# Optimization experiments

Hardware: AMD Instinct MI355X
Metric: run time of the kernel (lower is better)

## Reference

```python
import jax, jax.numpy as jnp
import numpy as np

EMBED = 1024
HEADS = 16
HEAD_DIM = EMBED // HEADS


def setup_inputs() -> dict:
    key = jax.random.key(0)
    ks = jax.random.split(key, 7)
    B, S = 2, 2048
    return {
        "key": jax.random.normal(ks[0], (B, S, EMBED), dtype=jnp.float32),
        "query": jax.random.normal(ks[1], (B, S, EMBED), dtype=jnp.float32),
        "value": jax.random.normal(ks[2], (B, S, EMBED), dtype=jnp.float32),
        "Wk": jax.random.normal(ks[3], (EMBED, EMBED), dtype=jnp.float32) * (EMBED ** -0.5),
        "Wq": jax.random.normal(ks[4], (EMBED, EMBED), dtype=jnp.float32) * (EMBED ** -0.5),
        "Wv": jax.random.normal(ks[5], (EMBED, EMBED), dtype=jnp.float32) * (EMBED ** -0.5),
        "Wo": jax.random.normal(ks[6], (EMBED, EMBED), dtype=jnp.float32) * (EMBED ** -0.5),
        "mask": 1,
    }


def _split_heads(x):
    B, S, _ = x.shape
    return x.reshape(B, S, HEADS, HEAD_DIM).transpose(0, 2, 1, 3)  # (B,H,S,D)


def reference(key, query, value, Wk, Wq, Wv, Wo, mask):
    # torch Linear (no bias): y = x @ W.T
    k = _split_heads(key @ Wk.T)
    q = _split_heads(query @ Wq.T)
    v = _split_heads(value @ Wv.T)
    # NOTE: module scales by sqrt(embed_dims), not sqrt(head_dims)
    scale = 1.0 / jnp.sqrt(jnp.float32(EMBED))
    scores = jnp.einsum('bhqd,bhkd->bhqk', q, k) * scale  # (B,H,S,S)
    S = scores.shape[-1]
    if mask:
        # triu(full(-100000), diagonal=1).type(int) -> exactly -100000 above diag
        causal = jnp.triu(jnp.full((S, S), -100000.0, dtype=jnp.float32), k=1)
        scores = scores + causal
    attn = jax.nn.softmax(scores, axis=-1)
    out = jnp.einsum('bhqk,bhkd->bhqd', attn, v)  # (B,H,S,D)
    B = out.shape[0]
    out = out.transpose(0, 2, 1, 3).reshape(B, S, EMBED)
    return out @ Wo.T
```

## Files before the change

kernel.cpp:

```cpp
#include <hip/hip_runtime.h>
#include <hip/hip_bf16.h>

typedef unsigned short u16;
typedef __attribute__((ext_vector_type(8))) short bf16x8;
typedef __attribute__((ext_vector_type(4))) float f32x4;

#define GLDS16(g, l)                                                        \
  __builtin_amdgcn_global_load_lds(                                         \
      (const __attribute__((address_space(1))) void*)(g),                   \
      (__attribute__((address_space(3))) void*)(l), 16, 0, 0)

__device__ __forceinline__ u16 f2bf(float f) {
  union { float f; unsigned u; } v; v.f = f;
  unsigned r = v.u + 0x7FFFu + ((v.u >> 16) & 1u);
  return (u16)(r >> 16);
}

__global__ __launch_bounds__(256) void cvt_kernel(const float4* __restrict__ in,
                                                  ushort4* __restrict__ out) {
  int i = blockIdx.x * 256 + threadIdx.x;
  float4 v = in[i];
  ushort4 o;
  o.x = f2bf(v.x); o.y = f2bf(v.y); o.z = f2bf(v.z); o.w = f2bf(v.w);
  out[i] = o;
}

template <int MODE>
__device__ __forceinline__ void gemm_core(const u16* __restrict__ A,
                                          const u16* __restrict__ W,
                                          void* __restrict__ C) {
  const int K = 1024;
  __shared__ u16 lds_a[4096];
  __shared__ u16 lds_b[4096];
  const int bn = blockIdx.x, bm = blockIdx.y;
  const int tid = threadIdx.x, l = tid & 63, wid = tid >> 6;
  const int wr = wid >> 1, wc = wid & 1;
  const int l4 = l >> 4, l15 = l & 15;

  f32x4 zero4 = {0.f, 0.f, 0.f, 0.f};
  f32x4 acc[4][4];
  for (int i = 0; i < 4; ++i)
    for (int j = 0; j < 4; ++j) acc[i][j] = zero4;

  const int srow = tid >> 2, scol = (tid & 3) * 8;
  const u16* Ag = A + (bm * 128 + srow) * K + scol;
  const u16* Wg = W + (bn * 128 + srow) * K + scol;
  char* la = (char*)lds_a + wid * 1024;
  char* lb = (char*)lds_b + wid * 1024;

  for (int kt = 0; kt < K; kt += 32) {
    GLDS16(Ag + kt, la);
    GLDS16(Ag + 64 * K + kt, la + 4096);
    GLDS16(Wg + kt, lb);
    GLDS16(Wg + 64 * K + kt, lb + 4096);
    __syncthreads();
    bf16x8 af[4], bf[4];
    for (int i = 0; i < 4; ++i)
      af[i] = *(const bf16x8*)((const char*)lds_a +
                               (wr * 64 + i * 16 + l15) * 64 + l4 * 16);
    for (int j = 0; j < 4; ++j)
      bf[j] = *(const bf16x8*)((const char*)lds_b +
                               (wc * 64 + j * 16 + l15) * 64 + l4 * 16);
    for (int i = 0; i < 4; ++i)
      for (int j = 0; j < 4; ++j)
        acc[i][j] = __builtin_amdgcn_mfma_f32_16x16x32_bf16(af[i], bf[j],
                                                            acc[i][j], 0, 0, 0);
    __syncthreads();
  }

  for (int i = 0; i < 4; ++i)
    for (int j = 0; j < 4; ++j) {
      f32x4 a = acc[i][j];
      for (int r = 0; r < 4; ++r) {
        int m = bm * 128 + wr * 64 + i * 16 + l4 * 4 + r;
        int n = bn * 128 + wc * 64 + j * 16 + l15;
        if (MODE == 0) {
          int bb = m >> 11, srw = m & 2047, h = n >> 6, d = n & 63;
          ((u16*)C)[((bb * 16 + h) * 2048 + srw) * 64 + d] = f2bf(a[r]);
        } else {
          ((float*)C)[m * 1024 + n] = a[r];
        }
      }
    }
}

__global__ __launch_bounds__(256) void gemm_proj(
    const u16* __restrict__ X0, const u16* __restrict__ X1,
    const u16* __restrict__ X2, const u16* __restrict__ W0,
    const u16* __restrict__ W1, const u16* __restrict__ W2,
    u16* __restrict__ O0, u16* __restrict__ O1, u16* __restrict__ O2) {
  int z = blockIdx.z;
  const u16* A = (z == 0) ? X0 : (z == 1) ? X1 : X2;
  const u16* W = (z == 0) ? W0 : (z == 1) ? W1 : W2;
  u16* O = (z == 0) ? O0 : (z == 1) ? O1 : O2;
  gemm_core<0>(A, W, (void*)O);
}

__global__ __launch_bounds__(256) void gemm_out(const u16* __restrict__ A,
                                                const u16* __restrict__ W,
                                                float* __restrict__ C) {
  gemm_core<1>(A, W, (void*)C);
}

__global__ __launch_bounds__(256) void transpose_v(const u16* __restrict__ Vp,
                                                   u16* __restrict__ Vt) {
  const int st = blockIdx.x, bh = blockIdx.y;
  const int d = threadIdx.x & 63, sg = threadIdx.x >> 6;
  const u16* src = Vp + bh * 131072;
  u16* dst = Vt + bh * 131072;
  const int s0 = st * 64 + sg * 16;
  u16 tmp[16];
  for (int i = 0; i < 16; ++i) tmp[i] = src[(s0 + i) * 64 + d];
  ushort4* o = (ushort4*)(dst + d * 2048 + s0);
  for (int k = 0; k < 4; ++k) {
    ushort4 t4;
    t4.x = tmp[4 * k]; t4.y = tmp[4 * k + 1];
    t4.z = tmp[4 * k + 2]; t4.w = tmp[4 * k + 3];
    o[k] = t4;
  }
}

__global__ __launch_bounds__(256) void attn_kernel(const u16* __restrict__ Qp,
                                                   const u16* __restrict__ Kp,
                                                   const u16* __restrict__ Vt,
                                                   u16* __restrict__ ctx) {
  const int x = blockIdx.x, bh = blockIdx.y;
  const int tid = threadIdx.x, w = tid >> 6, l = tid & 63;
  const int l4 = l >> 4, l15 = l & 15;
  __shared__ u16 lds_p[4][1024];
  char* pw = (char*)lds_p[w];

  const u16* Qbh = Qp + bh * 131072;
  const u16* Kbh = Kp + bh * 131072;
  const u16* Vbh = Vt + bh * 131072;
  const int b = bh >> 4, h = bh & 15;
  u16* ctxb = ctx + (size_t)b * 2048 * 1024 + h * 64;

  const float SCALE2 = 0.03125f * 1.44269504f;
  const float PEN2 = 144269.5f;
  const int swz = (l15 & 7) << 4;

  for (int half = 0; half < 2; ++half) {
    const int qt = half ? (31 - x) : x;
    const int q0 = qt * 64 + w * 16;

    const u16* qb = Qbh + (q0 + l15) * 64 + l4 * 8;
    const bf16x8 bq0 = *(const bf16x8*)(qb);
    const bf16x8 bq1 = *(const bf16x8*)(qb + 32);

    f32x4 zero4 = {0.f, 0.f, 0.f, 0.f};
    f32x4 accO[4];
    for (int g = 0; g < 4; ++g) accO[g] = zero4;
    float m2 = -1.0e30f, lsum = 0.f;

    for (int t2 = 0; t2 <= qt; ++t2) {
      const int kv0 = t2 * 64;
      const u16* kb = Kbh + (kv0 + l15) * 64 + l4 * 8;
      f32x4 s[4];
      for (int g = 0; g < 4; ++g) {
        bf16x8 kf = *(const bf16x8*)(kb + g * 1024);
        s[g] = __builtin_amdgcn_mfma_f32_16x16x32_bf16(kf, bq0, zero4, 0, 0, 0);
      }
      for (int g = 0; g < 4; ++g) {
        bf16x8 kf = *(const bf16x8*)(kb + g * 1024 + 32);
        s[g] = __builtin_amdgcn_mfma_f32_16x16x32_bf16(kf, bq1, s[g], 0, 0, 0);
      }
      const u16* vb = Vbh + l15 * 2048 + kv0 + l4 * 8;
      bf16x8 vf[8];
      for (int g = 0; g < 4; ++g) {
        vf[g] = *(const bf16x8*)(vb + g * 16 * 2048);
        vf[g + 4] = *(const bf16x8*)(vb + g * 16 * 2048 + 32);
      }
      float sv[4][4];
      if (t2 == qt) {
        const int q = q0 + l15;
        for (int g = 0; g < 4; ++g)
          for (int r = 0; r < 4; ++r) {
            int kv = kv0 + g * 16 + l4 * 4 + r;
            sv[g][r] = s[g][r] * SCALE2 - (kv > q ? PEN2 : 0.f);
          }
      } else {
        for (int g = 0; g < 4; ++g)
          for (int r = 0; r < 4; ++r) sv[g][r] = s[g][r] * SCALE2;
      }
      float mx = sv[0][0];
      for (int g = 0; g < 4; ++g)
        for (int r = 0; r < 4; ++r) mx = fmaxf(mx, sv[g][r]);
      mx = fmaxf(mx, __shfl_xor(mx, 16));
      mx = fmaxf(mx, __shfl_xor(mx, 32));
      const float mnew = fmaxf(m2, mx);
      const float alpha = __builtin_exp2f(m2 - mnew);
      m2 = mnew;
      float p[4][4], rs = 0.f;
      for (int g = 0; g < 4; ++g)
        for (int r = 0; r < 4; ++r) {
          float e = __builtin_exp2f(sv[g][r] - mnew);
          p[g][r] = e;
          rs += e;
        }
      rs += __shfl_xor(rs, 16);
      rs += __shfl_xor(rs, 32);
      lsum = lsum * alpha + rs;
      float aR[4];
      for (int r = 0; r < 4; ++r) aR[r] = __shfl(alpha, l4 * 4 + r);
      for (int g = 0; g < 4; ++g) {
        f32x4 t = accO[g];
        t[0] *= aR[0]; t[1] *= aR[1]; t[2] *= aR[2]; t[3] *= aR[3];
        accO[g] = t;
      }
      for (int g = 0; g < 4; ++g) {
        ushort4 q4;
        q4.x = f2bf(p[g][0]); q4.y = f2bf(p[g][1]);
        q4.z = f2bf(p[g][2]); q4.w = f2bf(p[g][3]);
        int byte = (l15 * 128 + g * 32 + l4 * 8) ^ swz;
        *(ushort4*)(pw + byte) = q4;
      }
      bf16x8 pa0 = *(const bf16x8*)(pw + ((l15 * 128 + l4 * 16) ^ swz));
      bf16x8 pa1 = *(const bf16x8*)(pw + ((l15 * 128 + 64 + l4 * 16) ^ swz));
      for (int g = 0; g < 4; ++g)
        accO[g] = __builtin_amdgcn_mfma_f32_16x16x32_bf16(pa0, vf[g],
                                                          accO[g], 0, 0, 0);
      for (int g = 0; g < 4; ++g)
        accO[g] = __builtin_amdgcn_mfma_f32_16x16x32_bf16(pa1, vf[g + 4],
                                                          accO[g], 0, 0, 0);
    }
    float inv[4];
    for (int r = 0; r < 4; ++r) inv[r] = 1.f / __shfl(lsum, l4 * 4 + r);
    for (int r = 0; r < 4; ++r) {
      u16* orow = ctxb + (size_t)(q0 + l4 * 4 + r) * 1024;
      for (int g = 0; g < 4; ++g)
        orow[g * 16 + l15] = f2bf(accO[g][r] * inv[r]);
    }
  }
}

extern "C" void kernel_launch(void* const* d_in, const int* in_sizes, int n_in,
                              void* d_out, int out_size, void* d_ws,
                              size_t ws_size, hipStream_t stream) {
  (void)in_sizes; (void)n_in; (void)out_size; (void)ws_size;
  const float* key = (const float*)d_in[0];
  const float* query = (const float*)d_in[1];
  const float* value = (const float*)d_in[2];
  const float* Wk = (const float*)d_in[3];
  const float* Wq = (const float*)d_in[4];
  const float* Wv = (const float*)d_in[5];
  const float* Wo = (const float*)d_in[6];

  char* ws = (char*)d_ws;
  u16* keyb = (u16*)(ws + 0);
  u16* qryb = (u16*)(ws + 8388608);
  u16* valb = (u16*)(ws + 16777216);
  u16* Wkb  = (u16*)(ws + 25165824);
  u16* Wqb  = (u16*)(ws + 27262976);
  u16* Wvb  = (u16*)(ws + 29360128);
  u16* Wob  = (u16*)(ws + 31457280);
  u16* Kp   = (u16*)(ws + 33554432);
  u16* Qp   = (u16*)(ws + 41943040);
  u16* Vp   = (u16*)(ws + 50331648);
  u16* Vt   = (u16*)(ws + 58720256);
  u16* ctx  = (u16*)(ws + 67108864);

  cvt_kernel<<<4096, 256, 0, stream>>>((const float4*)key, (ushort4*)keyb);
  cvt_kernel<<<4096, 256, 0, stream>>>((const float4*)query, (ushort4*)qryb);
  cvt_kernel<<<4096, 256, 0, stream>>>((const float4*)value, (ushort4*)valb);
  cvt_kernel<<<1024, 256, 0, stream>>>((const float4*)Wk, (ushort4*)Wkb);
  cvt_kernel<<<1024, 256, 0, stream>>>((const float4*)Wq, (ushort4*)Wqb);
  cvt_kernel<<<1024, 256, 0, stream>>>((const float4*)Wv, (ushort4*)Wvb);
  cvt_kernel<<<1024, 256, 0, stream>>>((const float4*)Wo, (ushort4*)Wob);

  gemm_proj<<<dim3(8, 32, 3), 256, 0, stream>>>(keyb, qryb, valb, Wkb, Wqb,
                                                Wvb, Kp, Qp, Vp);
  transpose_v<<<dim3(32, 32), 256, 0, stream>>>(Vp, Vt);
  attn_kernel<<<dim3(16, 32), 256, 0, stream>>>(Qp, Kp, Vt, ctx);
  gemm_out<<<dim3(8, 32), 256, 0, stream>>>(ctx, Wob, (float*)d_out);
}
```

Before: 312.6 us.

## Prefetch next K/V tile in attention, remap blocks, merge conversion launches

The attention loop now loads the next KV tile's K and V fragments into a second register set while computing on the current one, so global-load latency overlaps the MFMA and softmax work. The grid is flattened to 1D and blocks are remapped so consecutive blocks spread across batch-heads, likely for XCD/L2 locality. Launch bounds add a minimum occupancy hint. The seven fp32-to-bf16 conversion launches are merged into one kernel to cut launch overhead. Double-buffered register fragments raise VGPR pressure, which may conflict with the occupancy hint and cause spills.

New measurement: 314.4 us. No clear change (+0.6%).

```diff
diff --git a/kernel.cpp b/kernel.cpp
--- a/kernel.cpp
+++ b/kernel.cpp
@@ -16,13 +16,28 @@
   return (u16)(r >> 16);
 }
 
-__global__ __launch_bounds__(256) void cvt_kernel(const float4* __restrict__ in,
-                                                  ushort4* __restrict__ out) {
-  int i = blockIdx.x * 256 + threadIdx.x;
-  float4 v = in[i];
+__global__ __launch_bounds__(256) void cvt_all(
+    const float4* __restrict__ a0, const float4* __restrict__ a1,
+    const float4* __restrict__ a2, const float4* __restrict__ a3,
+    const float4* __restrict__ a4, const float4* __restrict__ a5,
+    const float4* __restrict__ a6, ushort4* __restrict__ b0,
+    ushort4* __restrict__ b1, ushort4* __restrict__ b2,
+    ushort4* __restrict__ b3, ushort4* __restrict__ b4,
+    ushort4* __restrict__ b5, ushort4* __restrict__ b6) {
+  int bid = blockIdx.x;
+  const float4* s; ushort4* d; int off;
+  if (bid < 4096)       { s = a0; d = b0; off = bid; }
+  else if (bid < 8192)  { s = a1; d = b1; off = bid - 4096; }
+  else if (bid < 12288) { s = a2; d = b2; off = bid - 8192; }
+  else if (bid < 13312) { s = a3; d = b3; off = bid - 12288; }
+  else if (bid < 14336) { s = a4; d = b4; off = bid - 13312; }
+  else if (bid < 15360) { s = a5; d = b5; off = bid - 14336; }
+  else                  { s = a6; d = b6; off = bid - 15360; }
+  int i = off * 256 + threadIdx.x;
+  float4 v = s[i];
   ushort4 o;
   o.x = f2bf(v.x); o.y = f2bf(v.y); o.z = f2bf(v.z); o.w = f2bf(v.w);
-  out[i] = o;
+  d[i] = o;
 }
 
 template <int MODE>
@@ -120,11 +135,12 @@
   }
 }
 
-__global__ __launch_bounds__(256) void attn_kernel(const u16* __restrict__ Qp,
-                                                   const u16* __restrict__ Kp,
-                                                   const u16* __restrict__ Vt,
-                                                   u16* __restrict__ ctx) {
-  const int x = blockIdx.x, bh = blockIdx.y;
+__global__ __launch_bounds__(256, 2) void attn_kernel(
+    const u16* __restrict__ Qp, const u16* __restrict__ Kp,
+    const u16* __restrict__ Vt, u16* __restrict__ ctx) {
+  const int bid = blockIdx.x;
+  const int logical = ((bid & 7) << 6) | (bid >> 3);
+  const int x = logical & 15, bh = logical >> 4;
   const int tid = threadIdx.x, w = tid >> 6, l = tid & 63;
   const int l4 = l >> 4, l15 = l & 15;
   __shared__ u16 lds_p[4][1024];
@@ -140,6 +156,21 @@
   const float PEN2 = 144269.5f;
   const int swz = (l15 & 7) << 4;
 
+  auto LOADK = [&](bf16x8* kf, int t) {
+    const u16* kb = Kbh + (t * 64 + l15) * 64 + l4 * 8;
+    for (int g = 0; g < 4; ++g) {
+      kf[g] = *(const bf16x8*)(kb + g * 1024);
+      kf[g + 4] = *(const bf16x8*)(kb + g * 1024 + 32);
+    }
+  };
+  auto LOADV = [&](bf16x8* vf, int t) {
+    const u16* vb = Vbh + l15 * 2048 + t * 64 + l4 * 8;
+    for (int g = 0; g < 4; ++g) {
+      vf[g] = *(const bf16x8*)(vb + g * 16 * 2048);
+      vf[g + 4] = *(const bf16x8*)(vb + g * 16 * 2048 + 32);
+    }
+  };
+
   for (int half = 0; half < 2; ++half) {
     const int qt = half ? (31 - x) : x;
     const int q0 = qt * 64 + w * 16;
@@ -153,24 +184,15 @@
     for (int g = 0; g < 4; ++g) accO[g] = zero4;
     float m2 = -1.0e30f, lsum = 0.f;
 
-    for (int t2 = 0; t2 <= qt; ++t2) {
+    auto BODY = [&](const bf16x8* kf, const bf16x8* vf, int t2) {
       const int kv0 = t2 * 64;
-      const u16* kb = Kbh + (kv0 + l15) * 64 + l4 * 8;
       f32x4 s[4];
-      for (int g = 0; g < 4; ++g) {
-        bf16x8 kf = *(const bf16x8*)(kb + g * 1024);
-        s[g] = __builtin_amdgcn_mfma_f32_16x16x32_bf16(kf, bq0, zero4, 0, 0, 0);
-      }
-      for (int g = 0; g < 4; ++g) {
-        bf16x8 kf = *(const bf16x8*)(kb + g * 1024 + 32);
-        s[g] = __builtin_amdgcn_mfma_f32_16x16x32_bf16(kf, bq1, s[g], 0, 0, 0);
-      }
-      const u16* vb = Vbh + l15 * 2048 + kv0 + l4 * 8;
-      bf16x8 vf[8];
-      for (int g = 0; g < 4; ++g) {
-        vf[g] = *(const bf16x8*)(vb + g * 16 * 2048);
-        vf[g + 4] = *(const bf16x8*)(vb + g * 16 * 2048 + 32);
-      }
+      for (int g = 0; g < 4; ++g)
+        s[g] = __builtin_amdgcn_mfma_f32_16x16x32_bf16(kf[g], bq0, zero4,
+                                                       0, 0, 0);
+      for (int g = 0; g < 4; ++g)
+        s[g] = __builtin_amdgcn_mfma_f32_16x16x32_bf16(kf[g + 4], bq1, s[g],
+                                                       0, 0, 0);
       float sv[4][4];
       if (t2 == qt) {
         const int q = q0 + l15;
@@ -223,7 +245,20 @@
       for (int g = 0; g < 4; ++g)
         accO[g] = __builtin_amdgcn_mfma_f32_16x16x32_bf16(pa1, vf[g + 4],
                                                           accO[g], 0, 0, 0);
-    }
+    };
+
+    bf16x8 k0[8], v0[8], k1[8], v1[8];
+    LOADK(k0, 0); LOADV(v0, 0);
+    int t2 = 0;
+    while (true) {
+      if (t2 < qt) { LOADK(k1, t2 + 1); LOADV(v1, t2 + 1); }
+      BODY(k0, v0, t2);
+      if (++t2 > qt) break;
+      if (t2 < qt) { LOADK(k0, t2 + 1); LOADV(v0, t2 + 1); }
+      BODY(k1, v1, t2);
+      if (++t2 > qt) break;
+    }
+
     float inv[4];
     for (int r = 0; r < 4; ++r) inv[r] = 1.f / __shfl(lsum, l4 * 4 + r);
     for (int r = 0; r < 4; ++r) {
@@ -260,17 +295,15 @@
   u16* Vt   = (u16*)(ws + 58720256);
   u16* ctx  = (u16*)(ws + 67108864);
 
-  cvt_kernel<<<4096, 256, 0, stream>>>((const float4*)key, (ushort4*)keyb);
-  cvt_kernel<<<4096, 256, 0, stream>>>((const float4*)query, (ushort4*)qryb);
-  cvt_kernel<<<4096, 256, 0, stream>>>((const float4*)value, (ushort4*)valb);
-  cvt_kernel<<<1024, 256, 0, stream>>>((const float4*)Wk, (ushort4*)Wkb);
-  cvt_kernel<<<1024, 256, 0, stream>>>((const float4*)Wq, (ushort4*)Wqb);
-  cvt_kernel<<<1024, 256, 0, stream>>>((const float4*)Wv, (ushort4*)Wvb);
-  cvt_kernel<<<1024, 256, 0, stream>>>((const float4*)Wo, (ushort4*)Wob);
+  cvt_all<<<16384, 256, 0, stream>>>(
+      (const float4*)key, (const float4*)query, (const float4*)value,
+      (const float4*)Wk, (const float4*)Wq, (const float4*)Wv,
+      (const float4*)Wo, (ushort4*)keyb, (ushort4*)qryb, (ushort4*)valb,
+      (ushort4*)Wkb, (ushort4*)Wqb, (ushort4*)Wvb, (ushort4*)Wob);
 
   gemm_proj<<<dim3(8, 32, 3), 256, 0, stream>>>(keyb, qryb, valb, Wkb, Wqb,
                                                 Wvb, Kp, Qp, Vp);
   transpose_v<<<dim3(32, 32), 256, 0, stream>>>(Vp, Vt);
-  attn_kernel<<<dim3(16, 32), 256, 0, stream>>>(Qp, Kp, Vt, ctx);
+  attn_kernel<<<512, 256, 0, stream>>>(Qp, Kp, Vt, ctx);
   gemm_out<<<dim3(8, 32), 256, 0, stream>>>(ctx, Wob, (float*)d_out);
 }
```
